# Kernel optimization log

Measured on AMD Instinct MI355X. Metric: run time of the kernel, lower is better.

## Reference

```python
import jax, jax.numpy as jnp
import numpy as np

N_SUPPORT = 65536
N_QUERY = 65536
FEAT = 1024
EMBED = 512
WAYS = 256


def setup_inputs() -> dict:
    key = jax.random.key(0)
    k1, k2, k3, k4 = jax.random.split(key, 4)
    support_images = jax.random.normal(k1, (N_SUPPORT, FEAT), dtype=jnp.float32)
    query_images = jax.random.normal(k2, (N_QUERY, FEAT), dtype=jnp.float32)
    # deterministic labels so every one of the `ways` classes is non-empty
    labels = jnp.arange(N_SUPPORT, dtype=jnp.int32) % WAYS
    support_labels = jax.nn.one_hot(labels, WAYS, dtype=jnp.int32)  # one-hot, as in torch forward
    W = jax.random.normal(k3, (FEAT, EMBED), dtype=jnp.float32) / np.sqrt(FEAT).astype(np.float32)
    b = jax.random.normal(k4, (EMBED,), dtype=jnp.float32) * 0.01
    return {
        "support_images": support_images,
        "support_labels": support_labels,
        "query_images": query_images,
        "W": W,
        "b": b,
    }


def reference(support_images, support_labels, query_images, W, b):
    ways = support_labels.shape[1]
    labels = jnp.argmax(support_labels, axis=1)  # [N_support]

    # backbone: Linear(feat -> embed)
    z_support = support_images @ W + b  # [N_support, E]
    z_query = query_images @ W + b      # [N_query, E]

    # fused per-class mean (replaces the python loop over classes)
    sums = jax.ops.segment_sum(z_support, labels, num_segments=ways)          # [ways, E]
    counts = jax.ops.segment_sum(jnp.ones((z_support.shape[0],), z_support.dtype),
                                 labels, num_segments=ways)                   # [ways]
    z_proto = sums / counts[:, None]

    # scores = -cdist(z_query, z_proto)  (euclidean, p=2)
    q2 = jnp.sum(z_query * z_query, axis=1, keepdims=True)   # [Nq, 1]
    p2 = jnp.sum(z_proto * z_proto, axis=1)[None, :]          # [1, ways]
    d2 = q2 + p2 - 2.0 * (z_query @ z_proto.T)                # [Nq, ways]
    scores = -jnp.sqrt(jnp.maximum(d2, 0.0))

    return jax.nn.softmax(scores, axis=1)
```

## Files before the change

kernel.cpp:

```cpp
#include <hip/hip_runtime.h>
#include <stdint.h>

#define NSUP 65536
#define NQRY 65536
#define FEAT 1024
#define EMB  512
#define WAYS 256

typedef unsigned short u16;
typedef unsigned int   u32;
typedef __attribute__((ext_vector_type(8))) __bf16 bf16x8;
typedef __attribute__((ext_vector_type(4))) float  f32x4;

static __device__ __forceinline__ u16 f2bf(float f) {
    u32 u = __builtin_bit_cast(u32, f);
    u32 r = u + 0x7fffu + ((u >> 16) & 1u);
    return (u16)(r >> 16);
}

static __device__ __forceinline__ void gl_lds16(const void* g, void* l) {
    __builtin_amdgcn_global_load_lds((const __attribute__((address_space(1))) u32*)g,
                                     (__attribute__((address_space(3))) u32*)l,
                                     16, 0, 0);
}

static __device__ __forceinline__ int swz16(int r, int s) {
    return r * 32 + ((s ^ ((r >> 1) & 3)) * 8);
}

__global__ __launch_bounds__(256) void k0_transpose(const float* __restrict__ W,
                                                    u16* __restrict__ Wt,
                                                    int* __restrict__ icounts) {
    const int t = threadIdx.x;
    if (blockIdx.x == 0) icounts[t] = 0;
    __shared__ float tile[64][65];
    const int bx = blockIdx.x;
    const int k0 = (bx & 15) * 64;
    const int e0 = (bx >> 4) * 64;
#pragma unroll
    for (int i = 0; i < 16; ++i) {
        int idx = t + i * 256;
        int kk = idx >> 6, ee = idx & 63;
        tile[kk][ee] = W[(size_t)(k0 + kk) * EMB + e0 + ee];
    }
    __syncthreads();
#pragma unroll
    for (int i = 0; i < 16; ++i) {
        int idx = t + i * 256;
        int ee = idx >> 6, kk = idx & 63;
        Wt[(size_t)(e0 + ee) * FEAT + k0 + kk] = f2bf(tile[kk][ee]);
    }
}

__global__ __launch_bounds__(256) void k1a_labels(const int* __restrict__ sl,
                                                  int* __restrict__ labels,
                                                  int* __restrict__ icounts) {
    const int row = blockIdx.x * 4 + (threadIdx.x >> 6);
    const int lane = threadIdx.x & 63;
    const int4* p = (const int4*)(sl + (size_t)row * WAYS);
    int4 v = p[lane];
    int my = -1;
    if (v.x) my = lane * 4 + 0;
    if (v.y) my = lane * 4 + 1;
    if (v.z) my = lane * 4 + 2;
    if (v.w) my = lane * 4 + 3;
#pragma unroll
    for (int m = 32; m; m >>= 1) my = max(my, __shfl_xor(my, m));
    if (lane == 0) {
        labels[row] = my;
        atomicAdd(&icounts[my], 1);
    }
}

__global__ __launch_bounds__(256) void k1p_prefix(const int* __restrict__ icounts,
                                                  int* __restrict__ offs,
                                                  int* __restrict__ cursor,
                                                  float* __restrict__ countsF) {
    __shared__ int s[256];
    const int t = threadIdx.x;
    const int v = icounts[t];
    s[t] = v;
    __syncthreads();
    for (int d = 1; d < 256; d <<= 1) {
        int x = (t >= d) ? s[t - d] : 0;
        __syncthreads();
        s[t] += x;
        __syncthreads();
    }
    const int exc = s[t] - v;
    offs[t] = exc;
    cursor[t] = exc;
    countsF[t] = (float)v;
}

__global__ __launch_bounds__(256) void k1s_scatter(const int* __restrict__ labels,
                                                   int* __restrict__ cursor,
                                                   int* __restrict__ perm) {
    const int r = blockIdx.x * 256 + threadIdx.x;
    const int lb = labels[r];
    const int pos = atomicAdd(&cursor[lb], 1);
    perm[pos] = r;
}

__global__ __launch_bounds__(256) void k1c_classsum(const float* __restrict__ img,
                                                    const int* __restrict__ perm,
                                                    const int* __restrict__ offs,
                                                    const int* __restrict__ icounts,
                                                    float* __restrict__ sums) {
    const int c  = blockIdx.x >> 2;
    const int fs = blockIdx.x & 3;
    const int t  = threadIdx.x;
    const int base = offs[c];
    const int n    = icounts[c];
    const size_t fcol = (size_t)fs * 256 + t;
    float acc = 0.f;
    int i = 0;
    for (; i + 8 <= n; i += 8) {
        int rr[8];
#pragma unroll
        for (int u = 0; u < 8; ++u) rr[u] = perm[base + i + u];
        float v[8];
#pragma unroll
        for (int u = 0; u < 8; ++u) v[u] = img[(size_t)rr[u] * FEAT + fcol];
#pragma unroll
        for (int u = 0; u < 8; ++u) acc += v[u];
    }
    for (; i < n; ++i) acc += img[(size_t)perm[base + i] * FEAT + fcol];
    sums[(size_t)c * FEAT + fcol] = acc;
}

__global__ __launch_bounds__(512) void k2_proto(const float* __restrict__ sums,
                                                const float* __restrict__ counts,
                                                const float* __restrict__ W,
                                                u16* __restrict__ zpb,
                                                float* __restrict__ p2) {
    __shared__ float proto[FEAT];
    __shared__ float red[8];
    const int c = blockIdx.x, t = threadIdx.x;
    const float inv = 1.0f / counts[c];
    proto[t]       = sums[(size_t)c * FEAT + t] * inv;
    proto[t + 512] = sums[(size_t)c * FEAT + t + 512] * inv;
    __syncthreads();
    float a0 = 0.f, a1 = 0.f, a2 = 0.f, a3 = 0.f;
#pragma unroll 8
    for (int k = 0; k < FEAT; k += 4) {
        a0 += proto[k + 0] * W[(size_t)(k + 0) * EMB + t];
        a1 += proto[k + 1] * W[(size_t)(k + 1) * EMB + t];
        a2 += proto[k + 2] * W[(size_t)(k + 2) * EMB + t];
        a3 += proto[k + 3] * W[(size_t)(k + 3) * EMB + t];
    }
    float z = (a0 + a1) + (a2 + a3);
    zpb[(size_t)c * EMB + t] = f2bf(z);
    float sq = z * z;
#pragma unroll
    for (int m = 1; m < 64; m <<= 1) sq += __shfl_xor(sq, m);
    if ((t & 63) == 0) red[t >> 6] = sq;
    __syncthreads();
    if (t == 0) {
        float s = 0.f;
#pragma unroll
        for (int i = 0; i < 8; ++i) s += red[i];
        p2[c] = s;
    }
}

__global__ __launch_bounds__(512, 4) void k3_zq(const float* __restrict__ Q,
                                                const u16* __restrict__ Wt,
                                                u16* __restrict__ zq,
                                                float* __restrict__ q2h) {
    __shared__ u16 Asl[2][128 * 32];
    __shared__ u16 Bsl[2][256 * 32];
    __shared__ float q2l[4][128];
    const int t = threadIdx.x;
    const int lane = t & 63, wave = t >> 6;
    const int wm = wave >> 2, wn = wave & 3;
    const size_t row0 = (size_t)(blockIdx.x >> 1) * 128;
    const int half = blockIdx.x & 1;
    const int n0 = half * 256;

    const int ar = t >> 2, as = t & 3;
    const float* aptr = Q + (row0 + ar) * FEAT + as * 8;
    const int aw = swz16(ar, as);
    float af[8];

    auto loadA = [&](int ks) {
        const float4* p = (const float4*)(aptr + ks * 32);
        float4 x = p[0], y = p[1];
        af[0] = x.x; af[1] = x.y; af[2] = x.z; af[3] = x.w;
        af[4] = y.x; af[5] = y.y; af[6] = y.z; af[7] = y.w;
    };
    auto writeA = [&](int buf) {
        uint4 w;
        w.x = (u32)f2bf(af[0]) | ((u32)f2bf(af[1]) << 16);
        w.y = (u32)f2bf(af[2]) | ((u32)f2bf(af[3]) << 16);
        w.z = (u32)f2bf(af[4]) | ((u32)f2bf(af[5]) << 16);
        w.w = (u32)f2bf(af[6]) | ((u32)f2bf(af[7]) << 16);
        *(uint4*)&Asl[buf][aw] = w;
    };
    auto stageB = [&](int buf, int ks) {
#pragma unroll
        for (int p = 0; p < 2; ++p) {
            int gi = t + p * 512;
            int r = gi >> 2, cc = gi & 3;
            int s = cc ^ ((r >> 1) & 3);
            gl_lds16(Wt + (size_t)(n0 + r) * FEAT + ks * 32 + s * 8, &Bsl[buf][gi * 8]);
        }
    };

    f32x4 acc[4][4];
#pragma unroll
    for (int mt = 0; mt < 4; ++mt)
#pragma unroll
        for (int nt = 0; nt < 4; ++nt) acc[mt][nt] = f32x4{0.f, 0.f, 0.f, 0.f};

    stageB(0, 0);
    loadA(0);
    writeA(0);
    __syncthreads();

    const int L = lane & 15, g = lane >> 4;
    const int ard = swz16(wm * 64 + L, g);
    const int brd = swz16(wn * 64 + L, g);

    int cur = 0;
    for (int ks = 0; ks < 32; ++ks) {
        const int nxt = cur ^ 1;
        if (ks < 31) { stageB(nxt, ks + 1); loadA(ks + 1); }
        bf16x8 a[4], b[4];
#pragma unroll
        for (int mt = 0; mt < 4; ++mt) a[mt] = *(const bf16x8*)&Asl[cur][ard + mt * 512];
#pragma unroll
        for (int nt = 0; nt < 4; ++nt) b[nt] = *(const bf16x8*)&Bsl[cur][brd + nt * 512];
#pragma unroll
        for (int mt = 0; mt < 4; ++mt)
#pragma unroll
            for (int nt = 0; nt < 4; ++nt)
                acc[mt][nt] = __builtin_amdgcn_mfma_f32_16x16x32_bf16(a[mt], b[nt], acc[mt][nt], 0, 0, 0);
        if (ks < 31) writeA(nxt);
        __syncthreads();
        cur = nxt;
    }

    const int c = L;
#pragma unroll
    for (int mt = 0; mt < 4; ++mt) {
#pragma unroll
        for (int j = 0; j < 4; ++j) {
            const int rloc = wm * 64 + mt * 16 + g * 4 + j;
            const size_t r = row0 + rloc;
            float ss = 0.f;
#pragma unroll
            for (int nt = 0; nt < 4; ++nt) {
                float v = acc[mt][nt][j];
                ss += v * v;
                zq[r * EMB + n0 + wn * 64 + nt * 16 + c] = f2bf(v);
            }
#pragma unroll
            for (int m = 1; m < 16; m <<= 1) ss += __shfl_xor(ss, m);
            if (c == 0) q2l[wn][rloc] = ss;
        }
    }
    __syncthreads();
    if (t < 128)
        q2h[(size_t)half * NQRY + row0 + t] =
            (q2l[0][t] + q2l[1][t]) + (q2l[2][t] + q2l[3][t]);
}

__global__ __launch_bounds__(512, 4) void k4_scores(const u16* __restrict__ zq,
                                                    const u16* __restrict__ zp,
                                                    const float* __restrict__ q2h,
                                                    const float* __restrict__ p2,
                                                    float* __restrict__ out) {
    __shared__ u16 Asl[2][128 * 32];
    __shared__ u16 Bsl[2][256 * 32];
    __shared__ float p2l[WAYS];
    __shared__ float q2s[128];
    const int t = threadIdx.x;
    const int lane = t & 63, wave = t >> 6;
    const int wm = wave >> 2, wn = wave & 3;
    const size_t row0 = (size_t)blockIdx.x * 128;
    if (t < WAYS) p2l[t] = p2[t];
    if (t >= WAYS && t < WAYS + 128) {
        int r = t - WAYS;
        q2s[r] = q2h[row0 + r] + q2h[(size_t)NQRY + row0 + r];
    }

    auto stage = [&](int buf, int ks) {
        { int r = t >> 2, cc = t & 3;
          int s = cc ^ ((r >> 1) & 3);
          gl_lds16(zq + (row0 + r) * EMB + ks * 32 + s * 8, &Asl[buf][t * 8]); }
#pragma unroll
        for (int p = 0; p < 2; ++p) {
            int gi = t + p * 512;
            int r = gi >> 2, cc = gi & 3;
            int s = cc ^ ((r >> 1) & 3);
            gl_lds16(zp + (size_t)r * EMB + ks * 32 + s * 8, &Bsl[buf][gi * 8]);
        }
    };

    f32x4 acc[4][4];
#pragma unroll
    for (int mt = 0; mt < 4; ++mt)
#pragma unroll
        for (int nt = 0; nt < 4; ++nt) acc[mt][nt] = f32x4{0.f, 0.f, 0.f, 0.f};

    stage(0, 0);
    __syncthreads();

    const int L = lane & 15, g = lane >> 4;
    const int ard = swz16(wm * 64 + L, g);
    const int brd = swz16(wn * 64 + L, g);

    int cur = 0;
    for (int ks = 0; ks < 16; ++ks) {
        const int nxt = cur ^ 1;
        if (ks < 15) stage(nxt, ks + 1);
        bf16x8 a[4], b[4];
#pragma unroll
        for (int mt = 0; mt < 4; ++mt) a[mt] = *(const bf16x8*)&Asl[cur][ard + mt * 512];
#pragma unroll
        for (int nt = 0; nt < 4; ++nt) b[nt] = *(const bf16x8*)&Bsl[cur][brd + nt * 512];
#pragma unroll
        for (int mt = 0; mt < 4; ++mt)
#pragma unroll
            for (int nt = 0; nt < 4; ++nt)
                acc[mt][nt] = __builtin_amdgcn_mfma_f32_16x16x32_bf16(a[mt], b[nt], acc[mt][nt], 0, 0, 0);
        __syncthreads();
        cur = nxt;
    }

    float* rmax = (float*)&Asl[0][0];
    float* rsum = rmax + 512;
    const int c = L;

#pragma unroll
    for (int mt = 0; mt < 4; ++mt)
#pragma unroll
        for (int j = 0; j < 4; ++j) {
            const int rloc = wm * 64 + mt * 16 + g * 4 + j;
            const float qv = q2s[rloc];
            float m_ = -1e30f;
#pragma unroll
            for (int nt = 0; nt < 4; ++nt) {
                float d2 = qv + p2l[wn * 64 + nt * 16 + c] - 2.f * acc[mt][nt][j];
                float s = -sqrtf(fmaxf(d2, 0.f));
                acc[mt][nt][j] = s;
                m_ = fmaxf(m_, s);
            }
#pragma unroll
            for (int m = 1; m < 16; m <<= 1) m_ = fmaxf(m_, __shfl_xor(m_, m));
            if (c == 0) rmax[rloc * 4 + wn] = m_;
        }
    __syncthreads();
#pragma unroll
    for (int mt = 0; mt < 4; ++mt)
#pragma unroll
        for (int j = 0; j < 4; ++j) {
            const int rloc = wm * 64 + mt * 16 + g * 4 + j;
            float m4 = fmaxf(fmaxf(rmax[rloc * 4 + 0], rmax[rloc * 4 + 1]),
                             fmaxf(rmax[rloc * 4 + 2], rmax[rloc * 4 + 3]));
            float s_ = 0.f;
#pragma unroll
            for (int nt = 0; nt < 4; ++nt) {
                float e = __expf(acc[mt][nt][j] - m4);
                acc[mt][nt][j] = e;
                s_ += e;
            }
#pragma unroll
            for (int m = 1; m < 16; m <<= 1) s_ += __shfl_xor(s_, m);
            if (c == 0) rsum[rloc * 4 + wn] = s_;
        }
    __syncthreads();
#pragma unroll
    for (int mt = 0; mt < 4; ++mt)
#pragma unroll
        for (int j = 0; j < 4; ++j) {
            const int rloc = wm * 64 + mt * 16 + g * 4 + j;
            float inv = 1.f / ((rsum[rloc * 4 + 0] + rsum[rloc * 4 + 1]) +
                               (rsum[rloc * 4 + 2] + rsum[rloc * 4 + 3]));
#pragma unroll
            for (int nt = 0; nt < 4; ++nt)
                out[(row0 + rloc) * WAYS + wn * 64 + nt * 16 + c] = acc[mt][nt][j] * inv;
        }
}

extern "C" void kernel_launch(void* const* d_in, const int* in_sizes, int n_in,
                              void* d_out, int out_size, void* d_ws, size_t ws_size,
                              hipStream_t stream) {
    (void)in_sizes; (void)n_in; (void)out_size; (void)ws_size;
    const float* simg = (const float*)d_in[0];
    const int*   slab = (const int*)d_in[1];
    const float* qimg = (const float*)d_in[2];
    const float* W    = (const float*)d_in[3];
    float* out = (float*)d_out;
    char* ws = (char*)d_ws;

    int*   labels = (int*)  (ws + 0);
    int*   perm   = (int*)  (ws + 262144);
    int*   icounts= (int*)  (ws + 524288);
    int*   offs   = (int*)  (ws + 525312);
    int*   cursor = (int*)  (ws + 526336);
    float* countsF= (float*)(ws + 527360);
    float* sums   = (float*)(ws + 528384);
    float* p2     = (float*)(ws + 1576960);
    u16*   zpb    = (u16*)  (ws + 1577984);
    u16*   Wt     = (u16*)  (ws + 1840128);
    u16*   zq     = (u16*)  (ws + 2888704);
    float* q2h    = (float*)(ws + 69997568);


    k0_transpose <<<128,            256, 0, stream>>>(W, Wt, icounts);
    k1a_labels   <<<NSUP / 4,       256, 0, stream>>>(slab, labels, icounts);
    k1p_prefix   <<<1,              256, 0, stream>>>(icounts, offs, cursor, countsF);
    k1s_scatter  <<<NSUP / 256,     256, 0, stream>>>(labels, cursor, perm);
    k1c_classsum <<<WAYS * 4,       256, 0, stream>>>(simg, perm, offs, icounts, sums);
    k2_proto     <<<WAYS,           512, 0, stream>>>(sums, countsF, W, zpb, p2);
    k3_zq        <<<(NQRY/128) * 2, 512, 0, stream>>>(qimg, Wt, zq, q2h);
    k4_scores    <<<NQRY / 128,     512, 0, stream>>>(zq, zpb, q2h, p2, out);
}
```

Measured before the change: 373.3 us.

## Triple-buffer LDS in the query-embedding and score GEMMs with prefetch distance two

Moves both MFMA GEMM kernels from double to triple LDS buffering. Global-to-LDS loads are issued two k-steps ahead, with explicit vmcnt waits and a single barrier per step, so memory latency overlaps more compute and one barrier is removed from each iteration. The cost is more shared memory per block, so launch bounds drop from 4 to 2 blocks per CU, and the hand-placed waitcnt and barrier ordering is fragile.

```diff
diff --git a/kernel.cpp b/kernel.cpp
--- a/kernel.cpp
+++ b/kernel.cpp
@@ -164,81 +164,92 @@
     }
 }
 
-__global__ __launch_bounds__(512, 4) void k3_zq(const float* __restrict__ Q,
+__global__ __launch_bounds__(512, 2) void k3_zq(const float* __restrict__ Q,
                                                 const u16* __restrict__ Wt,
                                                 u16* __restrict__ zq,
                                                 float* __restrict__ q2h) {
-    __shared__ u16 Asl[2][128 * 32];
-    __shared__ u16 Bsl[2][256 * 32];
+    __shared__ u16 Asl[3][128 * 32];
+    __shared__ u16 Bsl[3][256 * 32];
     __shared__ float q2l[4][128];
     const int t = threadIdx.x;
     const int lane = t & 63, wave = t >> 6;
     const int wm = wave >> 2, wn = wave & 3;
     const size_t row0 = (size_t)(blockIdx.x >> 1) * 128;
-    const int half = blockIdx.x & 1;
-    const int n0 = half * 256;
+    const int n0 = (blockIdx.x & 1) * 256;
 
     const int ar = t >> 2, as = t & 3;
     const float* aptr = Q + (row0 + ar) * FEAT + as * 8;
     const int aw = swz16(ar, as);
-    float af[8];
-
-    auto loadA = [&](int ks) {
+
+    auto stageB = [&](int slot, int ks) {
+#pragma unroll
+        for (int p = 0; p < 2; ++p) {
+            int gi = t + p * 512;
+            int r = gi >> 2, cc = gi & 3;
+            int s = cc ^ ((r >> 1) & 3);
+            gl_lds16(Wt + (size_t)(n0 + r) * FEAT + ks * 32 + s * 8, &Bsl[slot][gi * 8]);
+        }
+    };
+    auto loadA = [&](int ks, float (&af)[8]) {
         const float4* p = (const float4*)(aptr + ks * 32);
         float4 x = p[0], y = p[1];
         af[0] = x.x; af[1] = x.y; af[2] = x.z; af[3] = x.w;
         af[4] = y.x; af[5] = y.y; af[6] = y.z; af[7] = y.w;
     };
-    auto writeA = [&](int buf) {
+    auto writeA = [&](int slot, const float (&af)[8]) {
         uint4 w;
         w.x = (u32)f2bf(af[0]) | ((u32)f2bf(af[1]) << 16);
         w.y = (u32)f2bf(af[2]) | ((u32)f2bf(af[3]) << 16);
         w.z = (u32)f2bf(af[4]) | ((u32)f2bf(af[5]) << 16);
         w.w = (u32)f2bf(af[6]) | ((u32)f2bf(af[7]) << 16);
-        *(uint4*)&Asl[buf][aw] = w;
+        *(uint4*)&Asl[slot][aw] = w;
     };
-    auto stageB = [&](int buf, int ks) {
-#pragma unroll
-        for (int p = 0; p < 2; ++p) {
-            int gi = t + p * 512;
-            int r = gi >> 2, cc = gi & 3;
-            int s = cc ^ ((r >> 1) & 3);
-            gl_lds16(Wt + (size_t)(n0 + r) * FEAT + ks * 32 + s * 8, &Bsl[buf][gi * 8]);
-        }
-    };
 
     f32x4 acc[4][4];
 #pragma unroll
     for (int mt = 0; mt < 4; ++mt)
 #pragma unroll
         for (int nt = 0; nt < 4; ++nt) acc[mt][nt] = f32x4{0.f, 0.f, 0.f, 0.f};
-
-    stageB(0, 0);
-    loadA(0);
-    writeA(0);
-    __syncthreads();
 
     const int L = lane & 15, g = lane >> 4;
     const int ard = swz16(wm * 64 + L, g);
     const int brd = swz16(wn * 64 + L, g);
 
-    int cur = 0;
-    for (int ks = 0; ks < 32; ++ks) {
-        const int nxt = cur ^ 1;
-        if (ks < 31) { stageB(nxt, ks + 1); loadA(ks + 1); }
+    float afA[8], afB[8];
+    stageB(0, 0); loadA(0, afA);
+    stageB(1, 1); loadA(1, afB);
+    asm volatile("s_waitcnt vmcnt(4)" ::: "memory");
+    writeA(0, afA);
+
+    auto step = [&](int T, const float (&cur)[8], float (&nxt)[8]) {
+        asm volatile("s_waitcnt lgkmcnt(0)" ::: "memory");
+        __builtin_amdgcn_s_barrier();
+        if (T + 2 < 32) {
+            stageB((T + 2) % 3, T + 2);
+            loadA(T + 2, nxt);
+            asm volatile("s_waitcnt vmcnt(4)" ::: "memory");
+        } else {
+            asm volatile("s_waitcnt vmcnt(0)" ::: "memory");
+        }
+        if (T + 1 < 32) writeA((T + 1) % 3, cur);
+        __builtin_amdgcn_sched_barrier(0);
+        const u16* As = &Asl[T % 3][0];
+        const u16* Bs = &Bsl[T % 3][0];
         bf16x8 a[4], b[4];
 #pragma unroll
-        for (int mt = 0; mt < 4; ++mt) a[mt] = *(const bf16x8*)&Asl[cur][ard + mt * 512];
-#pragma unroll
-        for (int nt = 0; nt < 4; ++nt) b[nt] = *(const bf16x8*)&Bsl[cur][brd + nt * 512];
+        for (int mt = 0; mt < 4; ++mt) a[mt] = *(const bf16x8*)&As[ard + mt * 512];
+#pragma unroll
+        for (int nt = 0; nt < 4; ++nt) b[nt] = *(const bf16x8*)&Bs[brd + nt * 512];
 #pragma unroll
         for (int mt = 0; mt < 4; ++mt)
 #pragma unroll
             for (int nt = 0; nt < 4; ++nt)
                 acc[mt][nt] = __builtin_amdgcn_mfma_f32_16x16x32_bf16(a[mt], b[nt], acc[mt][nt], 0, 0, 0);
-        if (ks < 31) writeA(nxt);
-        __syncthreads();
-        cur = nxt;
+    };
+
+    for (int tt = 0; tt < 32; tt += 2) {
+        step(tt,     afB, afA);
+        step(tt + 1, afA, afB);
     }
 
     const int c = L;
@@ -262,17 +273,17 @@
     }
     __syncthreads();
     if (t < 128)
-        q2h[(size_t)half * NQRY + row0 + t] =
+        q2h[(size_t)(blockIdx.x & 1) * NQRY + row0 + t] =
             (q2l[0][t] + q2l[1][t]) + (q2l[2][t] + q2l[3][t]);
 }
 
-__global__ __launch_bounds__(512, 4) void k4_scores(const u16* __restrict__ zq,
+__global__ __launch_bounds__(512, 2) void k4_scores(const u16* __restrict__ zq,
                                                     const u16* __restrict__ zp,
                                                     const float* __restrict__ q2h,
                                                     const float* __restrict__ p2,
                                                     float* __restrict__ out) {
-    __shared__ u16 Asl[2][128 * 32];
-    __shared__ u16 Bsl[2][256 * 32];
+    __shared__ u16 Asl[3][128 * 32];
+    __shared__ u16 Bsl[3][256 * 32];
     __shared__ float p2l[WAYS];
     __shared__ float q2s[128];
     const int t = threadIdx.x;
@@ -285,16 +296,16 @@
         q2s[r] = q2h[row0 + r] + q2h[(size_t)NQRY + row0 + r];
     }
 
-    auto stage = [&](int buf, int ks) {
+    auto stage = [&](int slot, int ks) {
         { int r = t >> 2, cc = t & 3;
           int s = cc ^ ((r >> 1) & 3);
-          gl_lds16(zq + (row0 + r) * EMB + ks * 32 + s * 8, &Asl[buf][t * 8]); }
+          gl_lds16(zq + (row0 + r) * EMB + ks * 32 + s * 8, &Asl[slot][t * 8]); }
 #pragma unroll
         for (int p = 0; p < 2; ++p) {
             int gi = t + p * 512;
             int r = gi >> 2, cc = gi & 3;
             int s = cc ^ ((r >> 1) & 3);
-            gl_lds16(zp + (size_t)r * EMB + ks * 32 + s * 8, &Bsl[buf][gi * 8]);
+            gl_lds16(zp + (size_t)r * EMB + ks * 32 + s * 8, &Bsl[slot][gi * 8]);
         }
     };
 
@@ -303,31 +314,37 @@
     for (int mt = 0; mt < 4; ++mt)
 #pragma unroll
         for (int nt = 0; nt < 4; ++nt) acc[mt][nt] = f32x4{0.f, 0.f, 0.f, 0.f};
-
-    stage(0, 0);
-    __syncthreads();
 
     const int L = lane & 15, g = lane >> 4;
     const int ard = swz16(wm * 64 + L, g);
     const int brd = swz16(wn * 64 + L, g);
 
-    int cur = 0;
-    for (int ks = 0; ks < 16; ++ks) {
-        const int nxt = cur ^ 1;
-        if (ks < 15) stage(nxt, ks + 1);
+    stage(0, 0);
+    stage(1, 1);
+
+    for (int T = 0; T < 16; ++T) {
+        __builtin_amdgcn_s_barrier();
+        if (T + 2 < 16) {
+            stage((T + 2) % 3, T + 2);
+            asm volatile("s_waitcnt vmcnt(3)" ::: "memory");
+        } else {
+            asm volatile("s_waitcnt vmcnt(0)" ::: "memory");
+        }
+        __builtin_amdgcn_sched_barrier(0);
+        const u16* As = &Asl[T % 3][0];
+        const u16* Bs = &Bsl[T % 3][0];
         bf16x8 a[4], b[4];
 #pragma unroll
-        for (int mt = 0; mt < 4; ++mt) a[mt] = *(const bf16x8*)&Asl[cur][ard + mt * 512];
-#pragma unroll
-        for (int nt = 0; nt < 4; ++nt) b[nt] = *(const bf16x8*)&Bsl[cur][brd + nt * 512];
+        for (int mt = 0; mt < 4; ++mt) a[mt] = *(const bf16x8*)&As[ard + mt * 512];
+#pragma unroll
+        for (int nt = 0; nt < 4; ++nt) b[nt] = *(const bf16x8*)&Bs[brd + nt * 512];
 #pragma unroll
         for (int mt = 0; mt < 4; ++mt)
 #pragma unroll
             for (int nt = 0; nt < 4; ++nt)
                 acc[mt][nt] = __builtin_amdgcn_mfma_f32_16x16x32_bf16(a[mt], b[nt], acc[mt][nt], 0, 0, 0);
-        __syncthreads();
-        cur = nxt;
-    }
+    }
+    __syncthreads();
 
     float* rmax = (float*)&Asl[0][0];
     float* rsum = rmax + 512;
@@ -408,7 +425,6 @@
     u16*   zq     = (u16*)  (ws + 2888704);
     float* q2h    = (float*)(ws + 69997568);
 
-
     k0_transpose <<<128,            256, 0, stream>>>(W, Wt, icounts);
     k1a_labels   <<<NSUP / 4,       256, 0, stream>>>(slab, labels, icounts);
     k1p_prefix   <<<1,              256, 0, stream>>>(icounts, offs, cursor, countsF);
```

New measurement: 437.8 us. 17.3% more time.

## Fuse query embedding GEMM with score GEMM and softmax in one kernel

Applied to the files above, without the earlier changes.

Merges k3_zq and k4_scores into a single kernel. Each 128-row block now computes the full 512-wide query embedding, keeps it in LDS as bf16, and then runs the prototype distance GEMM and softmax straight from LDS. This removes the global write and re-read of zq and q2h, as well as one launch. In exchange the accumulator tile doubles (4x8), occupancy bounds drop from 4 to 2 blocks, the second GEMM is single-buffered with a full vmcnt wait each step, and each block loads the whole Wt matrix.

```diff
diff --git a/kernel.cpp b/kernel.cpp
--- a/kernel.cpp
+++ b/kernel.cpp
@@ -26,6 +26,9 @@
 
 static __device__ __forceinline__ int swz16(int r, int s) {
     return r * 32 + ((s ^ ((r >> 1) & 3)) * 8);
+}
+static __device__ __forceinline__ int zidx(int r, int C) {
+    return r * 512 + (C & ~31) + ((((C >> 3) & 3) ^ ((r >> 1) & 3)) << 3) + (C & 7);
 }
 
 __global__ __launch_bounds__(256) void k0_transpose(const float* __restrict__ W,
@@ -164,19 +167,25 @@
     }
 }
 
-__global__ __launch_bounds__(512, 4) void k3_zq(const float* __restrict__ Q,
-                                                const u16* __restrict__ Wt,
-                                                u16* __restrict__ zq,
-                                                float* __restrict__ q2h) {
-    __shared__ u16 Asl[2][128 * 32];
-    __shared__ u16 Bsl[2][256 * 32];
+struct SMemP1 { u16 Asl[2][128 * 32]; u16 Bsl[2][512 * 32]; };
+struct SMemP2 { u16 z[128 * 512]; u16 zps[256 * 32]; float rmax[512]; float rsum[512]; };
+union SMemU { SMemP1 p1; SMemP2 p2; };
+
+__global__ __launch_bounds__(512, 2) void k34_fused(const float* __restrict__ Q,
+                                                    const u16* __restrict__ Wt,
+                                                    const u16* __restrict__ zpb,
+                                                    const float* __restrict__ p2,
+                                                    float* __restrict__ out) {
+    __shared__ SMemU smu;
     __shared__ float q2l[4][128];
+    __shared__ float q2f[128];
+    __shared__ float p2l[WAYS];
+
     const int t = threadIdx.x;
     const int lane = t & 63, wave = t >> 6;
     const int wm = wave >> 2, wn = wave & 3;
-    const size_t row0 = (size_t)(blockIdx.x >> 1) * 128;
-    const int half = blockIdx.x & 1;
-    const int n0 = half * 256;
+    const int L = lane & 15, g = lane >> 4;
+    const size_t row0 = (size_t)blockIdx.x * 128;
 
     const int ar = t >> 2, as = t & 3;
     const float* aptr = Q + (row0 + ar) * FEAT + as * 8;
@@ -195,156 +204,120 @@
         w.y = (u32)f2bf(af[2]) | ((u32)f2bf(af[3]) << 16);
         w.z = (u32)f2bf(af[4]) | ((u32)f2bf(af[5]) << 16);
         w.w = (u32)f2bf(af[6]) | ((u32)f2bf(af[7]) << 16);
-        *(uint4*)&Asl[buf][aw] = w;
+        *(uint4*)&smu.p1.Asl[buf][aw] = w;
     };
     auto stageB = [&](int buf, int ks) {
 #pragma unroll
-        for (int p = 0; p < 2; ++p) {
+        for (int p = 0; p < 4; ++p) {
             int gi = t + p * 512;
             int r = gi >> 2, cc = gi & 3;
             int s = cc ^ ((r >> 1) & 3);
-            gl_lds16(Wt + (size_t)(n0 + r) * FEAT + ks * 32 + s * 8, &Bsl[buf][gi * 8]);
+            gl_lds16(Wt + (size_t)r * FEAT + ks * 32 + s * 8, &smu.p1.Bsl[buf][gi * 8]);
         }
     };
 
-    f32x4 acc[4][4];
-#pragma unroll
-    for (int mt = 0; mt < 4; ++mt)
-#pragma unroll
-        for (int nt = 0; nt < 4; ++nt) acc[mt][nt] = f32x4{0.f, 0.f, 0.f, 0.f};
+    f32x4 acc[4][8];
+#pragma unroll
+    for (int mt = 0; mt < 4; ++mt)
+#pragma unroll
+        for (int nt = 0; nt < 8; ++nt) acc[mt][nt] = f32x4{0.f, 0.f, 0.f, 0.f};
 
     stageB(0, 0);
     loadA(0);
     writeA(0);
     __syncthreads();
 
-    const int L = lane & 15, g = lane >> 4;
     const int ard = swz16(wm * 64 + L, g);
-    const int brd = swz16(wn * 64 + L, g);
+    const int brd = swz16(wn * 128 + L, g);
 
     int cur = 0;
     for (int ks = 0; ks < 32; ++ks) {
         const int nxt = cur ^ 1;
         if (ks < 31) { stageB(nxt, ks + 1); loadA(ks + 1); }
-        bf16x8 a[4], b[4];
-#pragma unroll
-        for (int mt = 0; mt < 4; ++mt) a[mt] = *(const bf16x8*)&Asl[cur][ard + mt * 512];
-#pragma unroll
-        for (int nt = 0; nt < 4; ++nt) b[nt] = *(const bf16x8*)&Bsl[cur][brd + nt * 512];
+        bf16x8 a[4], b[8];
+#pragma unroll
+        for (int mt = 0; mt < 4; ++mt) a[mt] = *(const bf16x8*)&smu.p1.Asl[cur][ard + mt * 512];
+#pragma unroll
+        for (int nt = 0; nt < 8; ++nt) b[nt] = *(const bf16x8*)&smu.p1.Bsl[cur][brd + nt * 512];
 #pragma unroll
         for (int mt = 0; mt < 4; ++mt)
 #pragma unroll
-            for (int nt = 0; nt < 4; ++nt)
+            for (int nt = 0; nt < 8; ++nt)
                 acc[mt][nt] = __builtin_amdgcn_mfma_f32_16x16x32_bf16(a[mt], b[nt], acc[mt][nt], 0, 0, 0);
         if (ks < 31) writeA(nxt);
         __syncthreads();
         cur = nxt;
     }
 
+#pragma unroll
+    for (int mt = 0; mt < 4; ++mt) {
+#pragma unroll
+        for (int j = 0; j < 4; ++j) {
+            const int r = wm * 64 + mt * 16 + g * 4 + j;
+            float ss = 0.f;
+#pragma unroll
+            for (int nt = 0; nt < 8; ++nt) {
+                float v = acc[mt][nt][j];
+                ss += v * v;
+                smu.p2.z[zidx(r, wn * 128 + nt * 16 + L)] = f2bf(v);
+            }
+#pragma unroll
+            for (int m = 1; m < 16; m <<= 1) ss += __shfl_xor(ss, m);
+            if (L == 0) q2l[wn][r] = ss;
+        }
+    }
+    __syncthreads();
+    if (t < 128) q2f[t] = (q2l[0][t] + q2l[1][t]) + (q2l[2][t] + q2l[3][t]);
+    else if (t < 384) p2l[t - 128] = p2[t - 128];
+
+    f32x4 acc2[4][4];
+#pragma unroll
+    for (int mt = 0; mt < 4; ++mt)
+#pragma unroll
+        for (int nt = 0; nt < 4; ++nt) acc2[mt][nt] = f32x4{0.f, 0.f, 0.f, 0.f};
+
+    const int ard3 = (wm * 64 + L) * 512 + ((g ^ ((L >> 1) & 3)) << 3);
+    const int brd3 = swz16(wn * 64 + L, g);
+
+    for (int ks2 = 0; ks2 < 16; ++ks2) {
+        __syncthreads();
+#pragma unroll
+        for (int p = 0; p < 2; ++p) {
+            int gi = t + p * 512;
+            int w = gi >> 2, cc = gi & 3;
+            int s = cc ^ ((w >> 1) & 3);
+            gl_lds16(zpb + (size_t)w * EMB + ks2 * 32 + s * 8, &smu.p2.zps[gi * 8]);
+        }
+        asm volatile("s_waitcnt vmcnt(0)" ::: "memory");
+        __syncthreads();
+        bf16x8 a[4], b[4];
+#pragma unroll
+        for (int mt = 0; mt < 4; ++mt) a[mt] = *(const bf16x8*)&smu.p2.z[ard3 + mt * 8192 + ks2 * 32];
+#pragma unroll
+        for (int nt = 0; nt < 4; ++nt) b[nt] = *(const bf16x8*)&smu.p2.zps[brd3 + nt * 512];
+#pragma unroll
+        for (int mt = 0; mt < 4; ++mt)
+#pragma unroll
+            for (int nt = 0; nt < 4; ++nt)
+                acc2[mt][nt] = __builtin_amdgcn_mfma_f32_16x16x32_bf16(a[mt], b[nt], acc2[mt][nt], 0, 0, 0);
+    }
+
+    float* rmax = smu.p2.rmax;
+    float* rsum = smu.p2.rsum;
     const int c = L;
-#pragma unroll
-    for (int mt = 0; mt < 4; ++mt) {
+
+#pragma unroll
+    for (int mt = 0; mt < 4; ++mt)
 #pragma unroll
         for (int j = 0; j < 4; ++j) {
             const int rloc = wm * 64 + mt * 16 + g * 4 + j;
-            const size_t r = row0 + rloc;
-            float ss = 0.f;
+            const float qv = q2f[rloc];
+            float m_ = -1e30f;
 #pragma unroll
             for (int nt = 0; nt < 4; ++nt) {
-                float v = acc[mt][nt][j];
-                ss += v * v;
-                zq[r * EMB + n0 + wn * 64 + nt * 16 + c] = f2bf(v);
-            }
-#pragma unroll
-            for (int m = 1; m < 16; m <<= 1) ss += __shfl_xor(ss, m);
-            if (c == 0) q2l[wn][rloc] = ss;
-        }
-    }
-    __syncthreads();
-    if (t < 128)
-        q2h[(size_t)half * NQRY + row0 + t] =
-            (q2l[0][t] + q2l[1][t]) + (q2l[2][t] + q2l[3][t]);
-}
-
-__global__ __launch_bounds__(512, 4) void k4_scores(const u16* __restrict__ zq,
-                                                    const u16* __restrict__ zp,
-                                                    const float* __restrict__ q2h,
-                                                    const float* __restrict__ p2,
-                                                    float* __restrict__ out) {
-    __shared__ u16 Asl[2][128 * 32];
-    __shared__ u16 Bsl[2][256 * 32];
-    __shared__ float p2l[WAYS];
-    __shared__ float q2s[128];
-    const int t = threadIdx.x;
-    const int lane = t & 63, wave = t >> 6;
-    const int wm = wave >> 2, wn = wave & 3;
-    const size_t row0 = (size_t)blockIdx.x * 128;
-    if (t < WAYS) p2l[t] = p2[t];
-    if (t >= WAYS && t < WAYS + 128) {
-        int r = t - WAYS;
-        q2s[r] = q2h[row0 + r] + q2h[(size_t)NQRY + row0 + r];
-    }
-
-    auto stage = [&](int buf, int ks) {
-        { int r = t >> 2, cc = t & 3;
-          int s = cc ^ ((r >> 1) & 3);
-          gl_lds16(zq + (row0 + r) * EMB + ks * 32 + s * 8, &Asl[buf][t * 8]); }
-#pragma unroll
-        for (int p = 0; p < 2; ++p) {
-            int gi = t + p * 512;
-            int r = gi >> 2, cc = gi & 3;
-            int s = cc ^ ((r >> 1) & 3);
-            gl_lds16(zp + (size_t)r * EMB + ks * 32 + s * 8, &Bsl[buf][gi * 8]);
-        }
-    };
-
-    f32x4 acc[4][4];
-#pragma unroll
-    for (int mt = 0; mt < 4; ++mt)
-#pragma unroll
-        for (int nt = 0; nt < 4; ++nt) acc[mt][nt] = f32x4{0.f, 0.f, 0.f, 0.f};
-
-    stage(0, 0);
-    __syncthreads();
-
-    const int L = lane & 15, g = lane >> 4;
-    const int ard = swz16(wm * 64 + L, g);
-    const int brd = swz16(wn * 64 + L, g);
-
-    int cur = 0;
-    for (int ks = 0; ks < 16; ++ks) {
-        const int nxt = cur ^ 1;
-        if (ks < 15) stage(nxt, ks + 1);
-        bf16x8 a[4], b[4];
-#pragma unroll
-        for (int mt = 0; mt < 4; ++mt) a[mt] = *(const bf16x8*)&Asl[cur][ard + mt * 512];
-#pragma unroll
-        for (int nt = 0; nt < 4; ++nt) b[nt] = *(const bf16x8*)&Bsl[cur][brd + nt * 512];
-#pragma unroll
-        for (int mt = 0; mt < 4; ++mt)
-#pragma unroll
-            for (int nt = 0; nt < 4; ++nt)
-                acc[mt][nt] = __builtin_amdgcn_mfma_f32_16x16x32_bf16(a[mt], b[nt], acc[mt][nt], 0, 0, 0);
-        __syncthreads();
-        cur = nxt;
-    }
-
-    float* rmax = (float*)&Asl[0][0];
-    float* rsum = rmax + 512;
-    const int c = L;
-
-#pragma unroll
-    for (int mt = 0; mt < 4; ++mt)
-#pragma unroll
-        for (int j = 0; j < 4; ++j) {
-            const int rloc = wm * 64 + mt * 16 + g * 4 + j;
-            const float qv = q2s[rloc];
-            float m_ = -1e30f;
-#pragma unroll
-            for (int nt = 0; nt < 4; ++nt) {
-                float d2 = qv + p2l[wn * 64 + nt * 16 + c] - 2.f * acc[mt][nt][j];
+                float d2 = qv + p2l[wn * 64 + nt * 16 + c] - 2.f * acc2[mt][nt][j];
                 float s = -sqrtf(fmaxf(d2, 0.f));
-                acc[mt][nt][j] = s;
+                acc2[mt][nt][j] = s;
                 m_ = fmaxf(m_, s);
             }
 #pragma unroll
@@ -362,8 +335,8 @@
             float s_ = 0.f;
 #pragma unroll
             for (int nt = 0; nt < 4; ++nt) {
-                float e = __expf(acc[mt][nt][j] - m4);
-                acc[mt][nt][j] = e;
+                float e = __expf(acc2[mt][nt][j] - m4);
+                acc2[mt][nt][j] = e;
                 s_ += e;
             }
 #pragma unroll
@@ -380,7 +353,7 @@
                                (rsum[rloc * 4 + 2] + rsum[rloc * 4 + 3]));
 #pragma unroll
             for (int nt = 0; nt < 4; ++nt)
-                out[(row0 + rloc) * WAYS + wn * 64 + nt * 16 + c] = acc[mt][nt][j] * inv;
+                out[(row0 + rloc) * WAYS + wn * 64 + nt * 16 + c] = acc2[mt][nt][j] * inv;
         }
 }
 
@@ -405,16 +378,13 @@
     float* p2     = (float*)(ws + 1576960);
     u16*   zpb    = (u16*)  (ws + 1577984);
     u16*   Wt     = (u16*)  (ws + 1840128);
-    u16*   zq     = (u16*)  (ws + 2888704);
-    float* q2h    = (float*)(ws + 69997568);
-
-
-    k0_transpose <<<128,            256, 0, stream>>>(W, Wt, icounts);
-    k1a_labels   <<<NSUP / 4,       256, 0, stream>>>(slab, labels, icounts);
-    k1p_prefix   <<<1,              256, 0, stream>>>(icounts, offs, cursor, countsF);
-    k1s_scatter  <<<NSUP / 256,     256, 0, stream>>>(labels, cursor, perm);
-    k1c_classsum <<<WAYS * 4,       256, 0, stream>>>(simg, perm, offs, icounts, sums);
-    k2_proto     <<<WAYS,           512, 0, stream>>>(sums, countsF, W, zpb, p2);
-    k3_zq        <<<(NQRY/128) * 2, 512, 0, stream>>>(qimg, Wt, zq, q2h);
-    k4_scores    <<<NQRY / 128,     512, 0, stream>>>(zq, zpb, q2h, p2, out);
-}
+
+
+    k0_transpose <<<128,        256, 0, stream>>>(W, Wt, icounts);
+    k1a_labels   <<<NSUP / 4,   256, 0, stream>>>(slab, labels, icounts);
+    k1p_prefix   <<<1,          256, 0, stream>>>(icounts, offs, cursor, countsF);
+    k1s_scatter  <<<NSUP / 256, 256, 0, stream>>>(labels, cursor, perm);
+    k1c_classsum <<<WAYS * 4,   256, 0, stream>>>(simg, perm, offs, icounts, sums);
+    k2_proto     <<<WAYS,       512, 0, stream>>>(sums, countsF, W, zpb, p2);
+    k34_fused    <<<NQRY / 128, 512, 0, stream>>>(qimg, Wt, zpb, p2, out);
+}
```

Result: slower. 443.7 us (+18.9%).
